# Performance work log

Measured on AMD Instinct MI355X. Metric: run time of the kernel, lower is better.

Reference implementation:

```python
import jax, jax.numpy as jnp
import numpy as np

MUL = 128            # multiplicity of every irrep (128x0e node features)
LS = (0, 1, 2, 3)    # sh irreps 0e,1o,2e,3o
SH_DIMS = tuple(2 * l + 1 for l in LS)  # (1,3,5,7) -> total 16
RB = 8               # radial basis features
N_NODES, N_EDGES = 5000, 100000


def setup_inputs() -> dict:
    key = jax.random.key(0)
    ks = jax.random.split(key, 12)
    return {
        "node_features": jax.random.normal(ks[0], (N_NODES, MUL), jnp.float32),
        "sph_harmonics": jax.random.normal(ks[1], (N_EDGES, sum(SH_DIMS)), jnp.float32),
        "radial_basis": jax.random.uniform(ks[2], (N_EDGES, RB), jnp.float32),
        "edge_i": jax.random.randint(ks[3], (N_EDGES,), 0, N_NODES),  # central atoms
        "edge_j": jax.random.randint(ks[4], (N_EDGES,), 0, N_NODES),  # neighbours
        "W_pre": jax.random.normal(ks[5], (MUL, MUL), jnp.float32),
        "mlp_w0": jax.random.normal(ks[6], (RB, 64), jnp.float32),
        "mlp_w1": jax.random.normal(ks[7], (64, 64), jnp.float32),
        "mlp_w2": jax.random.normal(ks[8], (64, 64), jnp.float32),
        "mlp_w3": jax.random.normal(ks[9], (64, len(LS) * MUL), jnp.float32),
        "W_post": jax.random.normal(ks[10], (len(LS), MUL, MUL), jnp.float32),
    }


def _forward(node_features, sph, rb, edge_i, edge_j,
             W_pre, mlp_w0, mlp_w1, mlp_w2, mlp_w3, W_post):
    N = node_features.shape[0]
    inv = np.float32(1.0 / np.sqrt(MUL))
    # pre o3.Linear on 128x0e: dense mix of multiplicities, fan-in normalized
    x = (node_features @ W_pre) * inv                       # [N, MUL]
    nbr = x[edge_j]                                         # gather neighbours [E, MUL]
    # per-edge weight generator: SiLU hidden layers, linear last, no bias
    h = rb
    for w in (mlp_w0, mlp_w1, mlp_w2):
        h = jax.nn.silu((h @ w) * np.float32(1.0 / np.sqrt(w.shape[0])))
    w_edge = (h @ mlp_w3) * np.float32(1.0 / np.sqrt(mlp_w3.shape[0]))  # [E, 4*MUL]
    w_edge = w_edge.reshape(-1, len(LS), MUL)               # one weight chunk per CG path
    off = 0
    out_blocks = []
    for p, d in enumerate(SH_DIMS):
        Y = sph[:, off:off + d]; off += d                   # [E, d]
        m = (nbr * w_edge[:, p, :])[:, :, None] * Y[:, None, :]  # messages [E, MUL, d]
        # scatter-aggregate messages onto central atoms (sum aggregation)
        tot = jax.ops.segment_sum(m.reshape(m.shape[0], -1), edge_i, num_segments=N)
        tot = tot.reshape(N, MUL, d)
        # post o3.Linear: per-irrep dense mix of multiplicities
        out_blocks.append(jnp.einsum('nud,uv->nvd', tot, W_post[p]) * inv)
    # reshape_irreps: [N, MUL, 1+3+5+7] = [N, 128, 16]
    return jnp.concatenate(out_blocks, axis=-1)


def reference(node_features, sph_harmonics, radial_basis, edge_i, edge_j,
              W_pre, mlp_w0, mlp_w1, mlp_w2, mlp_w3, W_post):
    return _forward(node_features, sph_harmonics, radial_basis, edge_i, edge_j,
                    W_pre, mlp_w0, mlp_w1, mlp_w2, mlp_w3, W_post)
```

## Files before the change

kernel.cpp:

```cpp
#include <hip/hip_runtime.h>
#include <hip/hip_bf16.h>

#define NN 5000
#define NE 100000

typedef unsigned short u16;
typedef __attribute__((ext_vector_type(8))) short bf16x8;
typedef __attribute__((ext_vector_type(4))) float f32x4;

__device__ __forceinline__ float silu_f(float x) {
    return x / (1.0f + __expf(-x));
}

__device__ __forceinline__ u16 f2bf(float x) {
    unsigned int u = __float_as_uint(x);
    u += 0x7FFFu + ((u >> 16) & 1u);
    return (u16)(u >> 16);
}
__device__ __forceinline__ float bf2f(u16 h) {
    return __uint_as_float(((unsigned int)h) << 16);
}

__global__ __launch_bounds__(128) void k_pre(const float* __restrict__ nf,
                                             const float* __restrict__ Wpre,
                                             float* __restrict__ x) {
    __shared__ float row[128];
    int n = blockIdx.x;
    int v = threadIdx.x;
    row[v] = nf[(size_t)n * 128 + v];
    __syncthreads();
    float acc = 0.f;
#pragma unroll 16
    for (int u = 0; u < 128; ++u) acc += row[u] * Wpre[u * 128 + v];
    x[(size_t)n * 128 + v] = acc * 0.08838834764831845f;
}

__global__ void k_count(const int* __restrict__ ei, int* __restrict__ counts) {
    int e = blockIdx.x * blockDim.x + threadIdx.x;
    if (e < NE) atomicAdd(&counts[ei[e]], 1);
}

__global__ __launch_bounds__(256) void k_scan(const int* __restrict__ counts,
                                              int* __restrict__ offsets) {
    __shared__ int part[256];
    int t = threadIdx.x;
    const int CH = 20;
    int lo = t * CH, hi = min(lo + CH, NN);
    int s = 0;
    for (int i = lo; i < hi; ++i) s += counts[i];
    part[t] = s;
    __syncthreads();
    if (t == 0) {
        int run = 0;
        for (int i = 0; i < 256; ++i) { int v = part[i]; part[i] = run; run += v; }
    }
    __syncthreads();
    int run = part[t];
    for (int i = lo; i < hi; ++i) { offsets[i] = run; run += counts[i]; }
    if (t == 0) offsets[NN] = NE;
}

__global__ void k_fill(const int* __restrict__ ei, const int* __restrict__ offsets,
                       int* __restrict__ cursor, int* __restrict__ order) {
    int e = blockIdx.x * blockDim.x + threadIdx.x;
    if (e < NE) {
        int i = ei[e];
        int pos = atomicAdd(&cursor[i], 1);
        order[offsets[i] + pos] = e;
    }
}

__global__ __launch_bounds__(256) void k_wprep(const float* __restrict__ w1,
                                               const float* __restrict__ w2,
                                               const float* __restrict__ w3,
                                               u16* __restrict__ w1h, u16* __restrict__ w1l,
                                               u16* __restrict__ w2h, u16* __restrict__ w2l,
                                               u16* __restrict__ w3h, u16* __restrict__ w3l) {
    int i = blockIdx.x * 256 + threadIdx.x;
    if (i < 4096) {
        int k = i >> 6, n = i & 63;
        float v = w1[i];
        u16 h = f2bf(v), l = f2bf(v - bf2f(h));
        w1h[n * 64 + k] = h; w1l[n * 64 + k] = l;
        v = w2[i];
        h = f2bf(v); l = f2bf(v - bf2f(h));
        w2h[n * 64 + k] = h; w2l[n * 64 + k] = l;
    }
    if (i < 32768) {
        int k = i >> 9, n = i & 511;
        float v = w3[i];
        u16 h = f2bf(v), l = f2bf(v - bf2f(h));
        w3h[n * 64 + k] = h; w3l[n * 64 + k] = l;
    }
}


__device__ __forceinline__ void layer_mid(const char* sh, const char* sl,
                                          const u16* __restrict__ wh,
                                          const u16* __restrict__ wl,
                                          char* dh, char* dl, int w, int l) {
    const int col = w * 16 + (l & 15);
    bf16x8 B[2][2];
#pragma unroll
    for (int kc = 0; kc < 2; ++kc) {
        B[kc][0] = *(const bf16x8*)(wh + col * 64 + kc * 32 + ((l >> 4) << 3));
        B[kc][1] = *(const bf16x8*)(wl + col * 64 + kc * 32 + ((l >> 4) << 3));
    }
#pragma unroll
    for (int rt = 0; rt < 4; ++rt) {
        const int arow = rt * 16 + (l & 15);
        f32x4 acc = {0.f, 0.f, 0.f, 0.f};
#pragma unroll
        for (int kc = 0; kc < 2; ++kc) {
            int off = (arow * 128 + kc * 64 + ((l >> 4) << 4)) ^ ((arow & 7) << 4);
            bf16x8 ah = *(const bf16x8*)(sh + off);
            bf16x8 al = *(const bf16x8*)(sl + off);
            acc = __builtin_amdgcn_mfma_f32_16x16x32_bf16(ah, B[kc][0], acc, 0, 0, 0);
            acc = __builtin_amdgcn_mfma_f32_16x16x32_bf16(ah, B[kc][1], acc, 0, 0, 0);
            acc = __builtin_amdgcn_mfma_f32_16x16x32_bf16(al, B[kc][0], acc, 0, 0, 0);
        }
#pragma unroll
        for (int r = 0; r < 4; ++r) {
            float v = silu_f(acc[r] * 0.125f);
            u16 hi = f2bf(v), lo = f2bf(v - bf2f(hi));
            int orow = rt * 16 + ((l >> 4) << 2) + r;
            int off = (orow * 128 + col * 2) ^ ((orow & 7) << 4);
            *(u16*)(dh + off) = hi;
            *(u16*)(dl + off) = lo;
        }
    }
}

__device__ __forceinline__ void layer_out(const char* sh, const char* sl,
                                          const u16* __restrict__ wh,
                                          const u16* __restrict__ wl,
                                          u16* __restrict__ we, int base, int w, int l) {
    const int r0 = (w & 1) * 32;
    const int c0 = (w >> 1) * 256;
    bf16x8 A[2][2][2];
#pragma unroll
    for (int rt = 0; rt < 2; ++rt)
#pragma unroll
        for (int kc = 0; kc < 2; ++kc) {
            int row = r0 + rt * 16 + (l & 15);
            int off = (row * 128 + kc * 64 + ((l >> 4) << 4)) ^ ((row & 7) << 4);
            A[rt][kc][0] = *(const bf16x8*)(sh + off);
            A[rt][kc][1] = *(const bf16x8*)(sl + off);
        }
    for (int nt = 0; nt < 16; ++nt) {
        const int col = c0 + nt * 16 + (l & 15);
        f32x4 acc[2] = {{0.f, 0.f, 0.f, 0.f}, {0.f, 0.f, 0.f, 0.f}};
#pragma unroll
        for (int kc = 0; kc < 2; ++kc) {
            bf16x8 bh = *(const bf16x8*)(wh + col * 64 + kc * 32 + ((l >> 4) << 3));
            bf16x8 bl = *(const bf16x8*)(wl + col * 64 + kc * 32 + ((l >> 4) << 3));
#pragma unroll
            for (int rt = 0; rt < 2; ++rt) {
                acc[rt] = __builtin_amdgcn_mfma_f32_16x16x32_bf16(A[rt][kc][0], bh, acc[rt], 0, 0, 0);
                acc[rt] = __builtin_amdgcn_mfma_f32_16x16x32_bf16(A[rt][kc][0], bl, acc[rt], 0, 0, 0);
                acc[rt] = __builtin_amdgcn_mfma_f32_16x16x32_bf16(A[rt][kc][1], bh, acc[rt], 0, 0, 0);
            }
        }
#pragma unroll
        for (int rt = 0; rt < 2; ++rt)
#pragma unroll
            for (int r = 0; r < 4; ++r) {
                int row = r0 + rt * 16 + ((l >> 4) << 2) + r;
                int e = base + row;
                if (e < NE) we[(size_t)e * 512 + col] = f2bf(acc[rt][r] * 0.125f);
            }
    }
}

__global__ __launch_bounds__(256) void k_mlp(const float* __restrict__ rb,
                                             const float* __restrict__ w0,
                                             const u16* __restrict__ w1h, const u16* __restrict__ w1l,
                                             const u16* __restrict__ w2h, const u16* __restrict__ w2l,
                                             const u16* __restrict__ w3h, const u16* __restrict__ w3l,
                                             u16* __restrict__ we) {
    __shared__ __align__(16) char hAh[8192];
    __shared__ __align__(16) char hAl[8192];
    __shared__ __align__(16) char hBh[8192];
    __shared__ __align__(16) char hBl[8192];
    __shared__ float rbs[512];
    const int t = threadIdx.x;
    const int l = t & 63, w = t >> 6;
    const int base = blockIdx.x * 64;

    for (int i = t; i < 512; i += 256) {
        int e = base + (i >> 3);
        rbs[i] = (e < NE) ? rb[(size_t)e * 8 + (i & 7)] : 0.f;
    }
    __syncthreads();

    {
        const int m = t >> 2, n0 = (t & 3) * 16;
        float h[16];
#pragma unroll
        for (int nn = 0; nn < 16; ++nn) h[nn] = 0.f;
#pragma unroll
        for (int k = 0; k < 8; ++k) {
            float r = rbs[m * 8 + k];
            const float* wp = w0 + k * 64 + n0;
#pragma unroll
            for (int nn = 0; nn < 16; ++nn) h[nn] += r * wp[nn];
        }
#pragma unroll
        for (int nn = 0; nn < 16; ++nn) {
            float v = silu_f(h[nn] * 0.35355339059327373f);
            u16 hi = f2bf(v), lo = f2bf(v - bf2f(hi));
            int off = (m * 128 + (n0 + nn) * 2) ^ ((m & 7) << 4);
            *(u16*)(hAh + off) = hi;
            *(u16*)(hAl + off) = lo;
        }
    }
    __syncthreads();
    layer_mid(hAh, hAl, w1h, w1l, hBh, hBl, w, l);
    __syncthreads();
    layer_mid(hBh, hBl, w2h, w2l, hAh, hAl, w, l);
    __syncthreads();
    layer_out(hAh, hAl, w3h, w3l, we, base, w, l);
}

__global__ __launch_bounds__(256) void k_gather(const float* __restrict__ x,
                                                const u16* __restrict__ we,
                                                const float* __restrict__ sph,
                                                const int* __restrict__ ej,
                                                const int* __restrict__ offsets,
                                                const int* __restrict__ order,
                                                const float* __restrict__ Wpost,
                                                float* __restrict__ out) {
    __shared__ float tot[4 * 128 * 24];
    const int t = threadIdx.x;
    const int w = t >> 6, lane = t & 63;
    const int n = blockIdx.x;
    const int s0 = offsets[n], s1 = offsets[n + 1];

    float acc0[16] = {};
    float acc1[16] = {};

    const int PMAP[16] = {0,1,1,1, 2,2,2,2, 2,3,3,3, 3,3,3,3};

    for (int idx = s0 + w; idx < s1; idx += 4) {
        int e = order[idx];
        int j = ej[e];
        const float* xp = x + (size_t)j * 128;
        float xj0 = xp[lane];
        float xj1 = xp[lane + 64];
        const u16* wep = we + (size_t)e * 512;
        float a0[4], a1[4];
#pragma unroll
        for (int p = 0; p < 4; ++p) {
            a0[p] = xj0 * bf2f(wep[p * 128 + lane]);
            a1[p] = xj1 * bf2f(wep[p * 128 + 64 + lane]);
        }
        const float4* Y4 = (const float4*)(sph + (size_t)e * 16);
        float yv[16];
        ((float4*)yv)[0] = Y4[0];
        ((float4*)yv)[1] = Y4[1];
        ((float4*)yv)[2] = Y4[2];
        ((float4*)yv)[3] = Y4[3];
#pragma unroll
        for (int k = 0; k < 16; ++k) {
            acc0[k] += a0[PMAP[k]] * yv[k];
            acc1[k] += a1[PMAP[k]] * yv[k];
        }
    }

    float* tw = tot + w * 3072;
#pragma unroll
    for (int k = 0; k < 16; ++k) {
        tw[lane * 24 + k]        = acc0[k];
        tw[(lane + 64) * 24 + k] = acc1[k];
    }
    __syncthreads();

    for (int i = t; i < 2048; i += 256) {
        int u = i >> 4, k = i & 15;
        int a = u * 24 + k;
        tot[a] = tot[a] + tot[3072 + a] + tot[2 * 3072 + a] + tot[3 * 3072 + a];
    }
    __syncthreads();

    const int v = t & 127, kh = t >> 7;
    const float* W0 = Wpost + v;
    const float* W1 = Wpost + 16384 + v;
    const float* W2 = Wpost + 2 * 16384 + v;
    const float* W3 = Wpost + 3 * 16384 + v;
    float acc[8] = {};
    if (kh == 0) {
        for (int u = 0; u < 128; ++u) {
            float4 ta = *(const float4*)&tot[u * 24 + 0];
            float4 tb = *(const float4*)&tot[u * 24 + 4];
            float wa = W0[u * 128];
            float wb = W1[u * 128];
            float wc = W2[u * 128];
            acc[0] += wa * ta.x;
            acc[1] += wb * ta.y; acc[2] += wb * ta.z; acc[3] += wb * ta.w;
            acc[4] += wc * tb.x; acc[5] += wc * tb.y; acc[6] += wc * tb.z; acc[7] += wc * tb.w;
        }
    } else {
        for (int u = 0; u < 128; ++u) {
            float4 ta = *(const float4*)&tot[u * 24 + 8];
            float4 tb = *(const float4*)&tot[u * 24 + 12];
            float wc = W2[u * 128];
            float wd = W3[u * 128];
            acc[0] += wc * ta.x;
            acc[1] += wd * ta.y; acc[2] += wd * ta.z; acc[3] += wd * ta.w;
            acc[4] += wd * tb.x; acc[5] += wd * tb.y; acc[6] += wd * tb.z; acc[7] += wd * tb.w;
        }
    }
    float* op = out + (size_t)n * 2048 + v * 16 + kh * 8;
    const float inv = 0.08838834764831845f;
    float4 r0 = make_float4(acc[0] * inv, acc[1] * inv, acc[2] * inv, acc[3] * inv);
    float4 r1 = make_float4(acc[4] * inv, acc[5] * inv, acc[6] * inv, acc[7] * inv);
    *(float4*)op = r0;
    *(float4*)(op + 4) = r1;
}

extern "C" void kernel_launch(void* const* d_in, const int* in_sizes, int n_in,
                              void* d_out, int out_size, void* d_ws, size_t ws_size,
                              hipStream_t stream) {
    const float* nf    = (const float*)d_in[0];
    const float* sph   = (const float*)d_in[1];
    const float* rb    = (const float*)d_in[2];
    const int*   ei    = (const int*)d_in[3];
    const int*   ej    = (const int*)d_in[4];
    const float* Wpre  = (const float*)d_in[5];
    const float* w0    = (const float*)d_in[6];
    const float* w1    = (const float*)d_in[7];
    const float* w2    = (const float*)d_in[8];
    const float* w3    = (const float*)d_in[9];
    const float* Wpost = (const float*)d_in[10];
    float* out = (float*)d_out;

    char* ws = (char*)d_ws;
    const size_t OFF_X       = 0;
    const size_t OFF_WE      = 2560000;
    const size_t OFF_COUNTS  = 104960000;
    const size_t OFF_CURSOR  = 104980000;
    const size_t OFF_OFFSETS = 105000000;
    const size_t OFF_ORDER   = 105020032;
    const size_t OFF_W1H     = 105420032;
    const size_t OFF_W1L     = OFF_W1H + 8192;
    const size_t OFF_W2H     = OFF_W1L + 8192;
    const size_t OFF_W2L     = OFF_W2H + 8192;
    const size_t OFF_W3H     = OFF_W2L + 8192;
    const size_t OFF_W3L     = OFF_W3H + 65536;
    const size_t NEEDED      = OFF_W3L + 65536;
    if (ws_size < NEEDED) return;

    float* x       = (float*)(ws + OFF_X);
    u16*   we      = (u16*)(ws + OFF_WE);
    int*   counts  = (int*)(ws + OFF_COUNTS);
    int*   cursor  = (int*)(ws + OFF_CURSOR);
    int*   offsets = (int*)(ws + OFF_OFFSETS);
    int*   order   = (int*)(ws + OFF_ORDER);
    u16*   w1h = (u16*)(ws + OFF_W1H); u16* w1l = (u16*)(ws + OFF_W1L);
    u16*   w2h = (u16*)(ws + OFF_W2H); u16* w2l = (u16*)(ws + OFF_W2L);
    u16*   w3h = (u16*)(ws + OFF_W3H); u16* w3l = (u16*)(ws + OFF_W3L);

    (void)hipMemsetAsync(ws + OFF_COUNTS, 0, 40000, stream);

    k_count<<<(NE + 255) / 256, 256, 0, stream>>>(ei, counts);
    k_scan<<<1, 256, 0, stream>>>(counts, offsets);
    k_fill<<<(NE + 255) / 256, 256, 0, stream>>>(ei, offsets, cursor, order);
    k_wprep<<<128, 256, 0, stream>>>(w1, w2, w3, w1h, w1l, w2h, w2l, w3h, w3l);

    k_pre<<<NN, 128, 0, stream>>>(nf, Wpre, x);
    k_mlp<<<(NE + 63) / 64, 256, 0, stream>>>(rb, w0, w1h, w1l, w2h, w2l, w3h, w3l, we);
    k_gather<<<NN, 256, 0, stream>>>(x, we, sph, ej, offsets, order, Wpost, out);
}
```

Measured before the change: 261.2 us.

## Split gather and post-linear into MFMA kernel; reduce MLP split-bf16 precision

The MLP activations are now stored as a single bf16 instead of hi/lo pairs, which halves the shared memory and drops one MFMA per product. The per-edge weight output layout is interleaved so that each lane loads its four path weights with one vector load. The gather kernel now gives one wave per node with shuffle-broadcast edge indices and writes split-bf16 aggregates to global memory. A new k_post kernel performs the W_post mix with MFMA instead of scalar FMAs. This adds a roughly 40MB global round-trip and an extra launch, and the lower MLP precision may hurt accuracy.

```diff
diff --git a/kernel.cpp b/kernel.cpp
--- a/kernel.cpp
+++ b/kernel.cpp
@@ -94,17 +94,28 @@
     }
 }
 
-
-__device__ __forceinline__ void layer_mid(const char* sh, const char* sl,
+__global__ __launch_bounds__(256) void k_wpprep(const float* __restrict__ Wpost,
+                                                u16* __restrict__ wpth,
+                                                u16* __restrict__ wptl) {
+    int i = blockIdx.x * 256 + threadIdx.x;
+    int p = i >> 14, rem = i & 16383, u = rem >> 7, v = rem & 127;
+    float val = Wpost[i];
+    u16 h = f2bf(val), l = f2bf(val - bf2f(h));
+    int o = (p * 128 + v) * 128 + u;
+    wpth[o] = h; wptl[o] = l;
+}
+
+
+__device__ __forceinline__ void layer_mid(const char* s,
                                           const u16* __restrict__ wh,
                                           const u16* __restrict__ wl,
-                                          char* dh, char* dl, int w, int l) {
+                                          char* d, int w, int l) {
     const int col = w * 16 + (l & 15);
-    bf16x8 B[2][2];
+    bf16x8 Bh[2], Bl[2];
 #pragma unroll
     for (int kc = 0; kc < 2; ++kc) {
-        B[kc][0] = *(const bf16x8*)(wh + col * 64 + kc * 32 + ((l >> 4) << 3));
-        B[kc][1] = *(const bf16x8*)(wl + col * 64 + kc * 32 + ((l >> 4) << 3));
+        Bh[kc] = *(const bf16x8*)(wh + col * 64 + kc * 32 + ((l >> 4) << 3));
+        Bl[kc] = *(const bf16x8*)(wl + col * 64 + kc * 32 + ((l >> 4) << 3));
     }
 #pragma unroll
     for (int rt = 0; rt < 4; ++rt) {
@@ -113,39 +124,34 @@
 #pragma unroll
         for (int kc = 0; kc < 2; ++kc) {
             int off = (arow * 128 + kc * 64 + ((l >> 4) << 4)) ^ ((arow & 7) << 4);
-            bf16x8 ah = *(const bf16x8*)(sh + off);
-            bf16x8 al = *(const bf16x8*)(sl + off);
-            acc = __builtin_amdgcn_mfma_f32_16x16x32_bf16(ah, B[kc][0], acc, 0, 0, 0);
-            acc = __builtin_amdgcn_mfma_f32_16x16x32_bf16(ah, B[kc][1], acc, 0, 0, 0);
-            acc = __builtin_amdgcn_mfma_f32_16x16x32_bf16(al, B[kc][0], acc, 0, 0, 0);
+            bf16x8 a = *(const bf16x8*)(s + off);
+            acc = __builtin_amdgcn_mfma_f32_16x16x32_bf16(a, Bh[kc], acc, 0, 0, 0);
+            acc = __builtin_amdgcn_mfma_f32_16x16x32_bf16(a, Bl[kc], acc, 0, 0, 0);
         }
 #pragma unroll
         for (int r = 0; r < 4; ++r) {
             float v = silu_f(acc[r] * 0.125f);
-            u16 hi = f2bf(v), lo = f2bf(v - bf2f(hi));
             int orow = rt * 16 + ((l >> 4) << 2) + r;
             int off = (orow * 128 + col * 2) ^ ((orow & 7) << 4);
-            *(u16*)(dh + off) = hi;
-            *(u16*)(dl + off) = lo;
-        }
-    }
-}
-
-__device__ __forceinline__ void layer_out(const char* sh, const char* sl,
+            *(u16*)(d + off) = f2bf(v);
+        }
+    }
+}
+
+__device__ __forceinline__ void layer_out(const char* s,
                                           const u16* __restrict__ wh,
                                           const u16* __restrict__ wl,
                                           u16* __restrict__ we, int base, int w, int l) {
     const int r0 = (w & 1) * 32;
     const int c0 = (w >> 1) * 256;
-    bf16x8 A[2][2][2];
+    bf16x8 A[2][2];
 #pragma unroll
     for (int rt = 0; rt < 2; ++rt)
 #pragma unroll
         for (int kc = 0; kc < 2; ++kc) {
             int row = r0 + rt * 16 + (l & 15);
             int off = (row * 128 + kc * 64 + ((l >> 4) << 4)) ^ ((row & 7) << 4);
-            A[rt][kc][0] = *(const bf16x8*)(sh + off);
-            A[rt][kc][1] = *(const bf16x8*)(sl + off);
+            A[rt][kc] = *(const bf16x8*)(s + off);
         }
     for (int nt = 0; nt < 16; ++nt) {
         const int col = c0 + nt * 16 + (l & 15);
@@ -156,18 +162,18 @@
             bf16x8 bl = *(const bf16x8*)(wl + col * 64 + kc * 32 + ((l >> 4) << 3));
 #pragma unroll
             for (int rt = 0; rt < 2; ++rt) {
-                acc[rt] = __builtin_amdgcn_mfma_f32_16x16x32_bf16(A[rt][kc][0], bh, acc[rt], 0, 0, 0);
-                acc[rt] = __builtin_amdgcn_mfma_f32_16x16x32_bf16(A[rt][kc][0], bl, acc[rt], 0, 0, 0);
-                acc[rt] = __builtin_amdgcn_mfma_f32_16x16x32_bf16(A[rt][kc][1], bh, acc[rt], 0, 0, 0);
+                acc[rt] = __builtin_amdgcn_mfma_f32_16x16x32_bf16(A[rt][kc], bh, acc[rt], 0, 0, 0);
+                acc[rt] = __builtin_amdgcn_mfma_f32_16x16x32_bf16(A[rt][kc], bl, acc[rt], 0, 0, 0);
             }
         }
+        const int up = ((col & 127) << 2) + (col >> 7);
 #pragma unroll
         for (int rt = 0; rt < 2; ++rt)
 #pragma unroll
             for (int r = 0; r < 4; ++r) {
                 int row = r0 + rt * 16 + ((l >> 4) << 2) + r;
                 int e = base + row;
-                if (e < NE) we[(size_t)e * 512 + col] = f2bf(acc[rt][r] * 0.125f);
+                if (e < NE) we[(size_t)e * 512 + up] = f2bf(acc[rt][r] * 0.125f);
             }
     }
 }
@@ -178,10 +184,8 @@
                                              const u16* __restrict__ w2h, const u16* __restrict__ w2l,
                                              const u16* __restrict__ w3h, const u16* __restrict__ w3l,
                                              u16* __restrict__ we) {
-    __shared__ __align__(16) char hAh[8192];
-    __shared__ __align__(16) char hAl[8192];
-    __shared__ __align__(16) char hBh[8192];
-    __shared__ __align__(16) char hBl[8192];
+    __shared__ __align__(16) char hA[8192];
+    __shared__ __align__(16) char hB[8192];
     __shared__ float rbs[512];
     const int t = threadIdx.x;
     const int l = t & 63, w = t >> 6;
@@ -208,18 +212,16 @@
 #pragma unroll
         for (int nn = 0; nn < 16; ++nn) {
             float v = silu_f(h[nn] * 0.35355339059327373f);
-            u16 hi = f2bf(v), lo = f2bf(v - bf2f(hi));
             int off = (m * 128 + (n0 + nn) * 2) ^ ((m & 7) << 4);
-            *(u16*)(hAh + off) = hi;
-            *(u16*)(hAl + off) = lo;
-        }
-    }
-    __syncthreads();
-    layer_mid(hAh, hAl, w1h, w1l, hBh, hBl, w, l);
-    __syncthreads();
-    layer_mid(hBh, hBl, w2h, w2l, hAh, hAl, w, l);
-    __syncthreads();
-    layer_out(hAh, hAl, w3h, w3l, we, base, w, l);
+            *(u16*)(hA + off) = f2bf(v);
+        }
+    }
+    __syncthreads();
+    layer_mid(hA, w1h, w1l, hB, w, l);
+    __syncthreads();
+    layer_mid(hB, w2h, w2l, hA, w, l);
+    __syncthreads();
+    layer_out(hA, w3h, w3l, we, base, w, l);
 }
 
 __global__ __launch_bounds__(256) void k_gather(const float* __restrict__ x,
@@ -228,94 +230,113 @@
                                                 const int* __restrict__ ej,
                                                 const int* __restrict__ offsets,
                                                 const int* __restrict__ order,
-                                                const float* __restrict__ Wpost,
-                                                float* __restrict__ out) {
-    __shared__ float tot[4 * 128 * 24];
-    const int t = threadIdx.x;
-    const int w = t >> 6, lane = t & 63;
-    const int n = blockIdx.x;
+                                                u16* __restrict__ toth,
+                                                u16* __restrict__ totl) {
+    const int lane = threadIdx.x & 63;
+    const int n = blockIdx.x * 4 + (threadIdx.x >> 6);
+    if (n >= NN) return;
     const int s0 = offsets[n], s1 = offsets[n + 1];
 
     float acc0[16] = {};
     float acc1[16] = {};
-
     const int PMAP[16] = {0,1,1,1, 2,2,2,2, 2,3,3,3, 3,3,3,3};
 
-    for (int idx = s0 + w; idx < s1; idx += 4) {
-        int e = order[idx];
-        int j = ej[e];
-        const float* xp = x + (size_t)j * 128;
-        float xj0 = xp[lane];
-        float xj1 = xp[lane + 64];
-        const u16* wep = we + (size_t)e * 512;
-        float a0[4], a1[4];
-#pragma unroll
-        for (int p = 0; p < 4; ++p) {
-            a0[p] = xj0 * bf2f(wep[p * 128 + lane]);
-            a1[p] = xj1 * bf2f(wep[p * 128 + 64 + lane]);
-        }
-        const float4* Y4 = (const float4*)(sph + (size_t)e * 16);
-        float yv[16];
-        ((float4*)yv)[0] = Y4[0];
-        ((float4*)yv)[1] = Y4[1];
-        ((float4*)yv)[2] = Y4[2];
-        ((float4*)yv)[3] = Y4[3];
-#pragma unroll
-        for (int k = 0; k < 16; ++k) {
-            acc0[k] += a0[PMAP[k]] * yv[k];
-            acc1[k] += a1[PMAP[k]] * yv[k];
-        }
-    }
-
-    float* tw = tot + w * 3072;
+    for (int base = s0; base < s1; base += 64) {
+        int idx = base + lane;
+        int ev = (idx < s1) ? order[idx] : 0;
+        int jv = (idx < s1) ? ej[ev] : 0;
+        int cnt = min(64, s1 - base);
+        for (int i = 0; i < cnt; ++i) {
+            int e = __shfl(ev, i);
+            int j = __shfl(jv, i);
+            const float* xp = x + (size_t)j * 128;
+            float xj0 = xp[lane];
+            float xj1 = xp[lane + 64];
+            const u16* wep = we + (size_t)e * 512;
+            ushort4 w0v = *(const ushort4*)(wep + lane * 4);
+            ushort4 w1v = *(const ushort4*)(wep + (lane + 64) * 4);
+            float a0[4] = {xj0 * bf2f(w0v.x), xj0 * bf2f(w0v.y),
+                           xj0 * bf2f(w0v.z), xj0 * bf2f(w0v.w)};
+            float a1[4] = {xj1 * bf2f(w1v.x), xj1 * bf2f(w1v.y),
+                           xj1 * bf2f(w1v.z), xj1 * bf2f(w1v.w)};
+            const float4* Y4 = (const float4*)(sph + (size_t)e * 16);
+            float yv[16];
+            ((float4*)yv)[0] = Y4[0];
+            ((float4*)yv)[1] = Y4[1];
+            ((float4*)yv)[2] = Y4[2];
+            ((float4*)yv)[3] = Y4[3];
+#pragma unroll
+            for (int k = 0; k < 16; ++k) {
+                acc0[k] += a0[PMAP[k]] * yv[k];
+                acc1[k] += a1[PMAP[k]] * yv[k];
+            }
+        }
+    }
+
 #pragma unroll
     for (int k = 0; k < 16; ++k) {
-        tw[lane * 24 + k]        = acc0[k];
-        tw[(lane + 64) * 24 + k] = acc1[k];
-    }
-    __syncthreads();
-
-    for (int i = t; i < 2048; i += 256) {
-        int u = i >> 4, k = i & 15;
-        int a = u * 24 + k;
-        tot[a] = tot[a] + tot[3072 + a] + tot[2 * 3072 + a] + tot[3 * 3072 + a];
-    }
-    __syncthreads();
-
-    const int v = t & 127, kh = t >> 7;
-    const float* W0 = Wpost + v;
-    const float* W1 = Wpost + 16384 + v;
-    const float* W2 = Wpost + 2 * 16384 + v;
-    const float* W3 = Wpost + 3 * 16384 + v;
-    float acc[8] = {};
-    if (kh == 0) {
-        for (int u = 0; u < 128; ++u) {
-            float4 ta = *(const float4*)&tot[u * 24 + 0];
-            float4 tb = *(const float4*)&tot[u * 24 + 4];
-            float wa = W0[u * 128];
-            float wb = W1[u * 128];
-            float wc = W2[u * 128];
-            acc[0] += wa * ta.x;
-            acc[1] += wb * ta.y; acc[2] += wb * ta.z; acc[3] += wb * ta.w;
-            acc[4] += wc * tb.x; acc[5] += wc * tb.y; acc[6] += wc * tb.z; acc[7] += wc * tb.w;
-        }
-    } else {
-        for (int u = 0; u < 128; ++u) {
-            float4 ta = *(const float4*)&tot[u * 24 + 8];
-            float4 tb = *(const float4*)&tot[u * 24 + 12];
-            float wc = W2[u * 128];
-            float wd = W3[u * 128];
-            acc[0] += wc * ta.x;
-            acc[1] += wd * ta.y; acc[2] += wd * ta.z; acc[3] += wd * ta.w;
-            acc[4] += wd * tb.x; acc[5] += wd * tb.y; acc[6] += wd * tb.z; acc[7] += wd * tb.w;
-        }
-    }
-    float* op = out + (size_t)n * 2048 + v * 16 + kh * 8;
+        size_t o = ((size_t)n * 16 + k) * 128;
+        u16 h0 = f2bf(acc0[k]);
+        toth[o + lane] = h0;
+        totl[o + lane] = f2bf(acc0[k] - bf2f(h0));
+        u16 h1 = f2bf(acc1[k]);
+        toth[o + 64 + lane] = h1;
+        totl[o + 64 + lane] = f2bf(acc1[k] - bf2f(h1));
+    }
+}
+
+__global__ __launch_bounds__(256) void k_post(const u16* __restrict__ toth,
+                                              const u16* __restrict__ totl,
+                                              const u16* __restrict__ wpth,
+                                              const u16* __restrict__ wptl,
+                                              float* __restrict__ out) {
+    const int gw = (blockIdx.x * 256 + threadIdx.x) >> 6;
+    const int lane = threadIdx.x & 63;
+    const int n0 = gw * 4;
+    if (n0 >= NN) return;
+    const int l15 = lane & 15, lg = lane >> 4;
+    const int KSTART[4] = {0, 1, 4, 9};
+    const int DP[4]     = {1, 3, 5, 7};
     const float inv = 0.08838834764831845f;
-    float4 r0 = make_float4(acc[0] * inv, acc[1] * inv, acc[2] * inv, acc[3] * inv);
-    float4 r1 = make_float4(acc[4] * inv, acc[5] * inv, acc[6] * inv, acc[7] * inv);
-    *(float4*)op = r0;
-    *(float4*)(op + 4) = r1;
+
+    for (int p = 0; p < 4; ++p) {
+        const int kst = KSTART[p], dp = DP[p];
+        for (int vt = 0; vt < 8; ++vt) {
+            f32x4 acc[4] = {{0,0,0,0},{0,0,0,0},{0,0,0,0},{0,0,0,0}};
+#pragma unroll
+            for (int ks = 0; ks < 4; ++ks) {
+                size_t aoff = ((size_t)(p * 128 + vt * 16 + l15)) * 128 + ks * 32 + lg * 8;
+                bf16x8 Ah = *(const bf16x8*)(wpth + aoff);
+                bf16x8 Al = *(const bf16x8*)(wptl + aoff);
+#pragma unroll
+                for (int nb = 0; nb < 4; ++nb) {
+                    int n = n0 + nb;
+                    if (n < NN) {
+                        size_t boff = ((size_t)(n * 16 + kst + l15)) * 128 + ks * 32 + lg * 8;
+                        bf16x8 Bh = *(const bf16x8*)(toth + boff);
+                        bf16x8 Bl = *(const bf16x8*)(totl + boff);
+                        acc[nb] = __builtin_amdgcn_mfma_f32_16x16x32_bf16(Ah, Bh, acc[nb], 0, 0, 0);
+                        acc[nb] = __builtin_amdgcn_mfma_f32_16x16x32_bf16(Ah, Bl, acc[nb], 0, 0, 0);
+                        acc[nb] = __builtin_amdgcn_mfma_f32_16x16x32_bf16(Al, Bh, acc[nb], 0, 0, 0);
+                    }
+                }
+            }
+            if (l15 < dp) {
+                const int kg = kst + l15;
+#pragma unroll
+                for (int nb = 0; nb < 4; ++nb) {
+                    int n = n0 + nb;
+                    if (n < NN) {
+#pragma unroll
+                        for (int r = 0; r < 4; ++r) {
+                            int v = vt * 16 + lg * 4 + r;
+                            out[(size_t)n * 2048 + v * 16 + kg] = acc[nb][r] * inv;
+                        }
+                    }
+                }
+            }
+        }
+    }
 }
 
 extern "C" void kernel_launch(void* const* d_in, const int* in_sizes, int n_in,
@@ -347,7 +368,11 @@
     const size_t OFF_W2L     = OFF_W2H + 8192;
     const size_t OFF_W3H     = OFF_W2L + 8192;
     const size_t OFF_W3L     = OFF_W3H + 65536;
-    const size_t NEEDED      = OFF_W3L + 65536;
+    const size_t OFF_TOTH    = OFF_W3L + 65536;
+    const size_t OFF_TOTL    = OFF_TOTH + 20484096;
+    const size_t OFF_WPTH    = OFF_TOTL + 20484096;
+    const size_t OFF_WPTL    = OFF_WPTH + 131072;
+    const size_t NEEDED      = OFF_WPTL + 131072;
     if (ws_size < NEEDED) return;
 
     float* x       = (float*)(ws + OFF_X);
@@ -359,6 +384,10 @@
     u16*   w1h = (u16*)(ws + OFF_W1H); u16* w1l = (u16*)(ws + OFF_W1L);
     u16*   w2h = (u16*)(ws + OFF_W2H); u16* w2l = (u16*)(ws + OFF_W2L);
     u16*   w3h = (u16*)(ws + OFF_W3H); u16* w3l = (u16*)(ws + OFF_W3L);
+    u16*   toth = (u16*)(ws + OFF_TOTH);
+    u16*   totl = (u16*)(ws + OFF_TOTL);
+    u16*   wpth = (u16*)(ws + OFF_WPTH);
+    u16*   wptl = (u16*)(ws + OFF_WPTL);
 
     (void)hipMemsetAsync(ws + OFF_COUNTS, 0, 40000, stream);
 
@@ -366,8 +395,10 @@
     k_scan<<<1, 256, 0, stream>>>(counts, offsets);
     k_fill<<<(NE + 255) / 256, 256, 0, stream>>>(ei, offsets, cursor, order);
     k_wprep<<<128, 256, 0, stream>>>(w1, w2, w3, w1h, w1l, w2h, w2l, w3h, w3l);
+    k_wpprep<<<256, 256, 0, stream>>>(Wpost, wpth, wptl);
 
     k_pre<<<NN, 128, 0, stream>>>(nf, Wpre, x);
     k_mlp<<<(NE + 63) / 64, 256, 0, stream>>>(rb, w0, w1h, w1l, w2h, w2l, w3h, w3l, we);
-    k_gather<<<NN, 256, 0, stream>>>(x, we, sph, ej, offsets, order, Wpost, out);
-}
+    k_gather<<<(NN + 3) / 4, 256, 0, stream>>>(x, we, sph, ej, offsets, order, toth, totl);
+    k_post<<<313, 256, 0, stream>>>(toth, totl, wpth, wptl, out);
+}
```

New measurement: 329.1 us. 1.26x slower.
